# Performance work log

Hardware: AMD Instinct MI355X
Metric: run time of the kernel (lower is better)

## Reference

```python
import jax, jax.numpy as jnp
import numpy as np

# --- constants matching the torch module's default-camera / material / light setup ---
IMAGE_SIZE = 128
SCALE = 1.0
FOCAL = 12.0
R_MAT = jnp.array([[-1.0, 0.0, 0.0], [0.0, 1.0, 0.0], [0.0, 0.0, -1.0]], dtype=jnp.float32)
T_VEC = jnp.array([0.0, 0.0, 2.0 * SCALE], dtype=jnp.float32)
CAM_POS = jnp.array([0.0, 0.0, 2.0 * SCALE], dtype=jnp.float32)  # camera center in world coords
LIGHT_LOC = jnp.array([0.0, 1.0, 3.0], dtype=jnp.float32)
AMB_L, DIFF_L, SPEC_L = 0.5, 0.3, 0.2          # PointLights defaults
MAT_AMB, MAT_DIFF, MAT_SPEC = 1.0, 1.0, 0.6    # Materials(specular_color=0.6)
SHININESS = 10.0
TEXEL = jnp.array([142.0, 179.0, 247.0], dtype=jnp.float32) / 255.0  # uniform vertex color
BG = 1.0  # BlendParams background
EPS = 1e-8


def _normalize(v):
    return v / (jnp.linalg.norm(v, axis=-1, keepdims=True) + EPS)


def _render_one(verts, faces):
    """verts: [V,3] world space; faces: [F,3] int. Returns ([3,H,W] rgb*255, [1,H,W] alpha)."""
    H = W = IMAGE_SIZE
    # world -> view (PyTorch3D row-vector convention: x_view = x @ R + T)
    view = verts @ R_MAT + T_VEC              # [V,3]
    z = view[:, 2]                            # [V] view-space depth (>0 in front)
    ndc = FOCAL * view[:, :2] / z[:, None]    # [V,2] perspective projection to NDC
    tri = ndc[faces]                          # [F,3,2]
    tz = z[faces]                             # [F,3]

    # pixel centers in NDC (PyTorch3D: +x left, +y up)
    xs = 1.0 - (2.0 * jnp.arange(W) + 1.0) / W
    ys = 1.0 - (2.0 * jnp.arange(H) + 1.0) / H
    gy, gx = jnp.meshgrid(ys, xs, indexing='ij')
    px = gx.reshape(-1).astype(jnp.float32)   # [P]
    py = gy.reshape(-1).astype(jnp.float32)   # [P]

    v0, v1, v2 = tri[:, 0], tri[:, 1], tri[:, 2]   # [F,2]

    def edge(a, b):  # signed area cross(b-a, p-a) for all pixels -> [P,F]
        return ((b[:, 0] - a[:, 0])[None] * (py[:, None] - a[:, 1][None])
                - (b[:, 1] - a[:, 1])[None] * (px[:, None] - a[:, 0][None]))

    area = ((v1[:, 0] - v0[:, 0]) * (v2[:, 1] - v0[:, 1])
            - (v1[:, 1] - v0[:, 1]) * (v2[:, 0] - v0[:, 0]))   # [F]
    area_safe = jnp.where(jnp.abs(area) < EPS, EPS, area)
    b0 = edge(v1, v2) / area_safe             # [P,F]
    b1 = edge(v2, v0) / area_safe
    b2 = 1.0 - b0 - b1
    inside = (b0 >= 0) & (b1 >= 0) & (b2 >= 0) & (jnp.abs(area) > EPS)[None]

    # perspective-correct interpolated depth: z_pix = 1 / sum_i(b_i / z_i)
    S = b0 / tz[:, 0] + b1 / tz[:, 1] + b2 / tz[:, 2]
    depth = jnp.where(inside & (S > EPS), 1.0 / jnp.maximum(S, EPS), jnp.inf)
    fidx = jnp.argmin(depth, axis=1)          # [P] z-buffer winner (faces_per_pixel=1)
    hit = jnp.isfinite(jnp.min(depth, axis=1))

    # --- recompute barycentrics only for the winning face per pixel (cheap, [P]) ---
    f = faces[fidx]                           # [P,3]
    tv = ndc[f]                               # [P,3,2]
    tzp = z[f]                                # [P,3]
    a0, a1, a2 = tv[:, 0], tv[:, 1], tv[:, 2]

    def edge_p(a, b):
        return (b[:, 0] - a[:, 0]) * (py - a[:, 1]) - (b[:, 1] - a[:, 1]) * (px - a[:, 0])

    ar = (a1[:, 0] - a0[:, 0]) * (a2[:, 1] - a0[:, 1]) - (a1[:, 1] - a0[:, 1]) * (a2[:, 0] - a0[:, 0])
    ar = jnp.where(jnp.abs(ar) < EPS, EPS, ar)
    bb0 = edge_p(a1, a2) / ar
    bb1 = edge_p(a2, a0) / ar
    bb2 = 1.0 - bb0 - bb1
    w = jnp.stack([bb0 / tzp[:, 0], bb1 / tzp[:, 1], bb2 / tzp[:, 2]], axis=-1)
    pc = w / (jnp.sum(w, axis=-1, keepdims=True) + EPS)   # [P,3] perspective-correct barycentrics

    # --- vertex normals (world space) ---
    fv = verts[faces]                         # [F,3,3]
    fn = jnp.cross(fv[:, 1] - fv[:, 0], fv[:, 2] - fv[:, 0])  # [F,3]
    vn = (jnp.zeros_like(verts)
          .at[faces[:, 0]].add(fn)
          .at[faces[:, 1]].add(fn)
          .at[faces[:, 2]].add(fn))
    vn = _normalize(vn)

    # --- interpolate position/normal, Phong shade ---
    pos = jnp.einsum('pk,pkd->pd', pc, verts[f])   # [P,3]
    nrm = _normalize(jnp.einsum('pk,pkd->pd', pc, vn[f]))
    l = _normalize(LIGHT_LOC - pos)
    vdir = _normalize(CAM_POS - pos)
    ndl = jax.nn.relu(jnp.sum(nrm * l, axis=-1))          # [P]
    refl = 2.0 * jnp.sum(nrm * l, axis=-1, keepdims=True) * nrm - l
    spec_cos = jax.nn.relu(jnp.sum(refl * vdir, axis=-1))
    ambient = AMB_L * MAT_AMB
    diffuse = DIFF_L * MAT_DIFF * ndl
    specular = SPEC_L * MAT_SPEC * spec_cos ** SHININESS
    color = TEXEL[None] * (ambient + diffuse[:, None]) + specular[:, None]

    rgb = jnp.where(hit[:, None], color, BG)              # hard blend with white bg
    alpha = hit.astype(verts.dtype)
    img = rgb.reshape(H, W, 3).transpose(2, 0, 1) * 255.0  # [3,H,W]
    a = alpha.reshape(1, H, W)
    return img, a


def setup_inputs() -> dict:
    key = jax.random.key(0)
    k1, k2 = jax.random.split(key)
    B, V, F = 2, 1300, 2500
    vertices = jax.random.normal(k1, (B, V, 3), dtype=jnp.float32) * 0.05  # head-scale mesh near origin
    faces = jax.random.randint(k2, (F, 3), 0, V, dtype=jnp.int32)
    return {"vertices": vertices, "faces": faces}


def reference(vertices, faces):
    # ori_size == image_size, so the area-interpolation in the torch module is the identity.
    images, alphas = jax.lax.map(lambda v: _render_one(v, faces), vertices)
    return images, alphas
```

## Files before the change

kernel.cpp:

```cpp
#include <hip/hip_runtime.h>
#include <math.h>

#pragma clang fp contract(off)

#define IMG_H 128
#define IMG_W 128
#define HW (IMG_H * IMG_W)
#define NB 2
#define NV 1300
#define NF 2500
#define EPSF 1e-8f
#define NCHUNK 32
#define CHUNK ((NF + NCHUNK - 1) / NCHUNK)
#define NREG 128
#define NBLK (NREG * NB * NCHUNK)

#define OFF_FACE 31232
#define OFF_DBUF 351488

#define DINIT 0x7F800000FFFFFFFFull

__global__ __launch_bounds__(256) void k_face(const float* __restrict__ verts,
                                              const int* __restrict__ faces,
                                              float* __restrict__ vn,
                                              float4* __restrict__ face) {
    int i = blockIdx.x * 256 + threadIdx.x;
    if (i >= NB * NF) return;
    int b = i / NF;
    int f = i - b * NF;
    int i0 = faces[f * 3 + 0];
    int i1 = faces[f * 3 + 1];
    int i2 = faces[f * 3 + 2];
    const float* wv = verts + (size_t)b * NV * 3;
    float v0x = wv[i0 * 3 + 0], v0y = wv[i0 * 3 + 1], v0z = wv[i0 * 3 + 2];
    float v1x = wv[i1 * 3 + 0], v1y = wv[i1 * 3 + 1], v1z = wv[i1 * 3 + 2];
    float v2x = wv[i2 * 3 + 0], v2y = wv[i2 * 3 + 1], v2z = wv[i2 * 3 + 2];
    float z0 = 2.0f - v0z, z1 = 2.0f - v1z, z2 = 2.0f - v2z;
    float p0x = (12.0f * (-v0x)) / z0, p0y = (12.0f * v0y) / z0;
    float p1x = (12.0f * (-v1x)) / z1, p1y = (12.0f * v1y) / z1;
    float p2x = (12.0f * (-v2x)) / z2, p2y = (12.0f * v2y) / z2;

    float t1 = (p1x - p0x) * (p2y - p0y);
    float t2 = (p1y - p0y) * (p2x - p0x);
    float area = t1 - t2;
    float aabs = fabsf(area);
    float area_safe = (aabs < EPSF) ? EPSF : area;
    bool valid = aabs > EPSF;
    float minx, maxx, miny, maxy;
    if (valid) {
        minx = fminf(p0x, fminf(p1x, p2x)) - 1e-3f;
        maxx = fmaxf(p0x, fmaxf(p1x, p2x)) + 1e-3f;
        miny = fminf(p0y, fminf(p1y, p2y)) - 1e-3f;
        maxy = fmaxf(p0y, fmaxf(p1y, p2y)) + 1e-3f;
    } else {
        minx = 1e30f; maxx = -1e30f; miny = 1e30f; maxy = -1e30f;
    }
    int o = (b * NF + f) * 4;
    face[o + 0] = make_float4(p2x - p1x, p2y - p1y, p1x, p1y);
    face[o + 1] = make_float4(p0x - p2x, p0y - p2y, p2x, p2y);
    face[o + 2] = make_float4(area_safe, z0, z1, z2);
    face[o + 3] = make_float4(minx, maxx, miny, maxy);

    float ax = v1x - v0x, ay = v1y - v0y, az = v1z - v0z;
    float bx = v2x - v0x, by = v2y - v0y, bz = v2z - v0z;
    float fnx = ay * bz - az * by;
    float fny = az * bx - ax * bz;
    float fnz = ax * by - ay * bx;
    float* vnb = vn + (size_t)b * NV * 3;
    atomicAdd(&vnb[i0 * 3 + 0], fnx);
    atomicAdd(&vnb[i0 * 3 + 1], fny);
    atomicAdd(&vnb[i0 * 3 + 2], fnz);
    atomicAdd(&vnb[i1 * 3 + 0], fnx);
    atomicAdd(&vnb[i1 * 3 + 1], fny);
    atomicAdd(&vnb[i1 * 3 + 2], fnz);
    atomicAdd(&vnb[i2 * 3 + 0], fnx);
    atomicAdd(&vnb[i2 * 3 + 1], fny);
    atomicAdd(&vnb[i2 * 3 + 2], fnz);
}

__global__ __launch_bounds__(128) void k_raster(const float4* __restrict__ face,
                                                unsigned long long* __restrict__ dbuf) {
    __shared__ float4 sface[CHUNK * 4];
    __shared__ int sidx[CHUNK];
    __shared__ unsigned short swl[2][CHUNK];
    __shared__ int sbase[2];
    __shared__ int sbaseA[2];
    __shared__ int sbaseB[2];

    int bx = blockIdx.x;
    int chunk = bx & (NCHUNK - 1);
    int tmp = bx >> 5;
    int b = tmp & 1;
    int reg = tmp >> 1;
    int r0 = (reg >> 3) * 8;
    int c0 = (reg & 7) * 16;
    int f0 = chunk * CHUNK;
    int nf = NF - f0; if (nf > CHUNK) nf = CHUNK;

    float txmax   = 1.0f - (2.0f * (float)c0 + 1.0f) / 128.0f;
    float txmid_h = 1.0f - (2.0f * (float)(c0 + 7) + 1.0f) / 128.0f;
    float txmid_l = 1.0f - (2.0f * (float)(c0 + 8) + 1.0f) / 128.0f;
    float txmin   = 1.0f - (2.0f * (float)(c0 + 15) + 1.0f) / 128.0f;
    float tymax = 1.0f - (2.0f * (float)r0 + 1.0f) / 128.0f;
    float tymin = 1.0f - (2.0f * (float)(r0 + 7) + 1.0f) / 128.0f;

    const float4* fb = face + (size_t)b * NF * 4;
    int t = threadIdx.x;
    int wid = t >> 6, lid = t & 63;
    bool pass = false, pA = false, pB = false;
    float4 bb;
    if (t < nf) {
        bb = fb[(f0 + t) * 4 + 3];
        bool yok = (bb.w >= tymin) && (bb.z <= tymax);
        pA = yok && (bb.y >= txmid_h) && (bb.x <= txmax);
        pB = yok && (bb.y >= txmin) && (bb.x <= txmid_l);
        pass = pA || pB;
    }
    unsigned long long m  = __ballot(pass);
    unsigned long long mA = __ballot(pA);
    unsigned long long mB = __ballot(pB);
    if (lid == 0) {
        sbase[wid]  = __popcll(m);
        sbaseA[wid] = __popcll(mA);
        sbaseB[wid] = __popcll(mB);
    }
    __syncthreads();
    if (pass) {
        unsigned long long lt = (1ull << lid) - 1ull;
        int pos = (wid ? sbase[0] : 0) + __popcll(m & lt);
        sface[pos * 4 + 0] = fb[(f0 + t) * 4 + 0];
        sface[pos * 4 + 1] = fb[(f0 + t) * 4 + 1];
        sface[pos * 4 + 2] = fb[(f0 + t) * 4 + 2];
        sface[pos * 4 + 3] = bb;
        sidx[pos] = f0 + t;
        if (pA) swl[0][(wid ? sbaseA[0] : 0) + __popcll(mA & lt)] = (unsigned short)pos;
        if (pB) swl[1][(wid ? sbaseB[0] : 0) + __popcll(mB & lt)] = (unsigned short)pos;
    }
    __syncthreads();
    int cnt = wid ? (sbaseB[0] + sbaseB[1]) : (sbaseA[0] + sbaseA[1]);

    int r = r0 + (lid >> 3);
    int c = c0 + wid * 8 + (lid & 7);
    int p = r * IMG_W + c;
    float px = 1.0f - (2.0f * (float)c + 1.0f) / 128.0f;
    float py = 1.0f - (2.0f * (float)r + 1.0f) / 128.0f;

    unsigned long long best = DINIT;
    for (int j = 0; j < cnt; ++j) {
        int jj = swl[wid][j];
        float4 fbb = sface[jj * 4 + 3];
        if (px >= fbb.x && px <= fbb.y && py >= fbb.z && py <= fbb.w) {
            float4 E0 = sface[jj * 4 + 0];
            float4 E1 = sface[jj * 4 + 1];
            float4 FD = sface[jj * 4 + 2];
            float u1 = E0.x * (py - E0.w);
            float u2 = E0.y * (px - E0.z);
            float e0 = u1 - u2;
            float u3 = E1.x * (py - E1.w);
            float u4 = E1.y * (px - E1.z);
            float e1 = u3 - u4;
            float as = FD.x;
            bool ok = (as > 0.0f) ? (e0 >= 0.0f && e1 >= 0.0f)
                                  : (e0 <= 0.0f && e1 <= 0.0f);
            if (ok) {
                float b0 = e0 / as;
                float b1 = e1 / as;
                float b2 = (1.0f - b0) - b1;
                if (b2 >= 0.0f) {
                    float S = ((b0 / FD.y) + (b1 / FD.z)) + (b2 / FD.w);
                    if (S > EPSF) {
                        float depth = 1.0f / fmaxf(S, EPSF);
                        unsigned long long pk =
                            ((unsigned long long)__float_as_uint(depth) << 32) |
                            (unsigned)sidx[jj];
                        if (pk < best) best = pk;
                    }
                }
            }
        }
    }
    dbuf[((size_t)chunk * NB + b) * HW + p] = best;
}

__global__ __launch_bounds__(256) void k_shade(const float* __restrict__ verts,
                                               const int* __restrict__ faces,
                                               const float* __restrict__ vn,
                                               const unsigned long long* __restrict__ dbuf,
                                               float* __restrict__ out) {
    int i = blockIdx.x * 256 + threadIdx.x;
    int b = i >> 14;
    int p = i & (HW - 1);
    unsigned long long pk = DINIT;
    for (int k = 0; k < NCHUNK; ++k) {
        unsigned long long v = dbuf[((size_t)k * NB + b) * HW + p];
        if (v < pk) pk = v;
    }
    unsigned dbits = (unsigned)(pk >> 32);
    bool hit = dbits < 0x7F800000u;
    float cr = 255.0f, cg = 255.0f, cb = 255.0f, alpha = 0.0f;
    if (hit) {
        alpha = 1.0f;
        int f = (int)(unsigned)(pk & 0xFFFFFFFFull);
        int row = p >> 7;
        int col = p & 127;
        float px = 1.0f - (2.0f * (float)col + 1.0f) / 128.0f;
        float py = 1.0f - (2.0f * (float)row + 1.0f) / 128.0f;
        int i0 = faces[f * 3 + 0];
        int i1 = faces[f * 3 + 1];
        int i2 = faces[f * 3 + 2];
        const float* wv = verts + (size_t)b * NV * 3;
        float v0x = wv[i0 * 3 + 0], v0y = wv[i0 * 3 + 1], v0z = wv[i0 * 3 + 2];
        float v1x = wv[i1 * 3 + 0], v1y = wv[i1 * 3 + 1], v1z = wv[i1 * 3 + 2];
        float v2x = wv[i2 * 3 + 0], v2y = wv[i2 * 3 + 1], v2z = wv[i2 * 3 + 2];
        float z0 = 2.0f - v0z, z1 = 2.0f - v1z, z2 = 2.0f - v2z;
        float a0x = (12.0f * (-v0x)) / z0, a0y = (12.0f * v0y) / z0;
        float a1x = (12.0f * (-v1x)) / z1, a1y = (12.0f * v1y) / z1;
        float a2x = (12.0f * (-v2x)) / z2, a2y = (12.0f * v2y) / z2;

        float t1 = (a1x - a0x) * (a2y - a0y);
        float t2 = (a1y - a0y) * (a2x - a0x);
        float ar = t1 - t2;
        ar = (fabsf(ar) < EPSF) ? EPSF : ar;
        float u1 = (a2x - a1x) * (py - a1y);
        float u2 = (a2y - a1y) * (px - a1x);
        float bb0 = (u1 - u2) / ar;
        float u3 = (a0x - a2x) * (py - a2y);
        float u4 = (a0y - a2y) * (px - a2x);
        float bb1 = (u3 - u4) / ar;
        float bb2 = (1.0f - bb0) - bb1;
        float w0 = bb0 / z0;
        float w1 = bb1 / z1;
        float w2 = bb2 / z2;
        float denom = ((w0 + w1) + w2) + EPSF;
        float pc0 = w0 / denom;
        float pc1 = w1 / denom;
        float pc2 = w2 / denom;

        float posx = (pc0 * v0x + pc1 * v1x) + pc2 * v2x;
        float posy = (pc0 * v0y + pc1 * v1y) + pc2 * v2y;
        float posz = (pc0 * v0z + pc1 * v1z) + pc2 * v2z;

        const float* vnb = vn + (size_t)b * NV * 3;
        float n0x = vnb[i0 * 3 + 0], n0y = vnb[i0 * 3 + 1], n0z = vnb[i0 * 3 + 2];
        float n1x = vnb[i1 * 3 + 0], n1y = vnb[i1 * 3 + 1], n1z = vnb[i1 * 3 + 2];
        float n2x = vnb[i2 * 3 + 0], n2y = vnb[i2 * 3 + 1], n2z = vnb[i2 * 3 + 2];
        float in0 = 1.0f / (sqrtf(n0x * n0x + n0y * n0y + n0z * n0z) + EPSF);
        float in1 = 1.0f / (sqrtf(n1x * n1x + n1y * n1y + n1z * n1z) + EPSF);
        float in2 = 1.0f / (sqrtf(n2x * n2x + n2y * n2y + n2z * n2z) + EPSF);
        n0x *= in0; n0y *= in0; n0z *= in0;
        n1x *= in1; n1y *= in1; n1z *= in1;
        n2x *= in2; n2y *= in2; n2z *= in2;
        float nx = (pc0 * n0x + pc1 * n1x) + pc2 * n2x;
        float ny = (pc0 * n0y + pc1 * n1y) + pc2 * n2y;
        float nz = (pc0 * n0z + pc1 * n1z) + pc2 * n2z;
        float inn = 1.0f / (sqrtf(nx * nx + ny * ny + nz * nz) + EPSF);
        nx *= inn; ny *= inn; nz *= inn;

        float lx = 0.0f - posx, ly = 1.0f - posy, lz = 3.0f - posz;
        float iln = 1.0f / (sqrtf(lx * lx + ly * ly + lz * lz) + EPSF);
        lx *= iln; ly *= iln; lz *= iln;
        float vx = 0.0f - posx, vy = 0.0f - posy, vz = 2.0f - posz;
        float ivn = 1.0f / (sqrtf(vx * vx + vy * vy + vz * vz) + EPSF);
        vx *= ivn; vy *= ivn; vz *= ivn;

        float ndl = nx * lx + ny * ly + nz * lz;
        float ndlr = fmaxf(ndl, 0.0f);
        float rx = 2.0f * ndl * nx - lx;
        float ry = 2.0f * ndl * ny - ly;
        float rz = 2.0f * ndl * nz - lz;
        float sc = fmaxf(rx * vx + ry * vy + rz * vz, 0.0f);
        float spec = 0.2f * 0.6f * powf(sc, 10.0f);
        float shade = 0.5f * 1.0f + 0.3f * 1.0f * ndlr;
        cr = ((142.0f / 255.0f) * shade + spec) * 255.0f;
        cg = ((179.0f / 255.0f) * shade + spec) * 255.0f;
        cb = ((247.0f / 255.0f) * shade + spec) * 255.0f;
    }
    float* img = out + (size_t)b * 3 * HW;
    img[0 * HW + p] = cr;
    img[1 * HW + p] = cg;
    img[2 * HW + p] = cb;
    out[(size_t)NB * 3 * HW + (size_t)b * HW + p] = alpha;
}

extern "C" void kernel_launch(void* const* d_in, const int* in_sizes, int n_in,
                              void* d_out, int out_size, void* d_ws, size_t ws_size,
                              hipStream_t stream) {
    const float* verts = (const float*)d_in[0];
    const int* faces = (const int*)d_in[1];
    char* ws = (char*)d_ws;
    float* vn = (float*)(ws + 0);
    float4* face = (float4*)(ws + OFF_FACE);
    unsigned long long* dbuf = (unsigned long long*)(ws + OFF_DBUF);
    float* out = (float*)d_out;

    hipMemsetAsync(vn, 0, NB * NV * 3 * sizeof(float), stream);
    k_face<<<(NB * NF + 255) / 256, 256, 0, stream>>>(verts, faces, vn, face);
    k_raster<<<NBLK, 128, 0, stream>>>(face, dbuf);
    k_shade<<<(NB * HW) / 256, 256, 0, stream>>>(verts, faces, vn, dbuf, out);
}
```

Measured before the change: 104.1 us.

## Cull faces per tile with edge-function bounds and merge depths via atomicMin

Tightens per-tile face culling in the raster kernel. It evaluates edge-function bounds over each half-tile rectangle and drops faces whose triangle cannot overlap it, using a small tolerance. It also replaces the per-chunk depth buffer and the 32-way min reduction in the shade kernel with 64-bit atomicMin into a single buffer, initialised by an extra memset. This cuts shared-memory candidates, dbuf traffic and the shade reduction, at the cost of atomic contention and an extra memset launch.

```diff
diff --git a/kernel.cpp b/kernel.cpp
--- a/kernel.cpp
+++ b/kernel.cpp
@@ -18,7 +18,7 @@
 #define OFF_FACE 31232
 #define OFF_DBUF 351488
 
-#define DINIT 0x7F800000FFFFFFFFull
+#define DINIT 0xFFFFFFFFFFFFFFFFull
 
 __global__ __launch_bounds__(256) void k_face(const float* __restrict__ verts,
                                               const int* __restrict__ faces,
@@ -108,12 +108,45 @@
     int t = threadIdx.x;
     int wid = t >> 6, lid = t & 63;
     bool pass = false, pA = false, pB = false;
-    float4 bb;
+    float4 bb, E0, E1, FD;
     if (t < nf) {
         bb = fb[(f0 + t) * 4 + 3];
         bool yok = (bb.w >= tymin) && (bb.z <= tymax);
         pA = yok && (bb.y >= txmid_h) && (bb.x <= txmax);
         pB = yok && (bb.y >= txmin) && (bb.x <= txmid_l);
+        if (pA || pB) {
+            E0 = fb[(f0 + t) * 4 + 0];
+            E1 = fb[(f0 + t) * 4 + 1];
+            FD = fb[(f0 + t) * 4 + 2];
+            float as = FD.x;
+            float u0l = E0.x * (tymin - E0.w), u0h = E0.x * (tymax - E0.w);
+            float u0mn = fminf(u0l, u0h), u0mx = fmaxf(u0l, u0h);
+            float u1l = E1.x * (tymin - E1.w), u1h = E1.x * (tymax - E1.w);
+            float u1mn = fminf(u1l, u1h), u1mx = fmaxf(u1l, u1h);
+            float v0al = E0.y * (txmid_h - E0.z), v0ah = E0.y * (txmax - E0.z);
+            float v0amn = fminf(v0al, v0ah), v0amx = fmaxf(v0al, v0ah);
+            float v1al = E1.y * (txmid_h - E1.z), v1ah = E1.y * (txmax - E1.z);
+            float v1amn = fminf(v1al, v1ah), v1amx = fmaxf(v1al, v1ah);
+            float v0bl = E0.y * (txmin - E0.z), v0bh = E0.y * (txmid_l - E0.z);
+            float v0bmn = fminf(v0bl, v0bh), v0bmx = fmaxf(v0bl, v0bh);
+            float v1bl = E1.y * (txmin - E1.z), v1bh = E1.y * (txmid_l - E1.z);
+            float v1bmn = fminf(v1bl, v1bh), v1bmx = fmaxf(v1bl, v1bh);
+            float e0amx = u0mx - v0amn, e0amn = u0mn - v0amx;
+            float e1amx = u1mx - v1amn, e1amn = u1mn - v1amx;
+            float e0bmx = u0mx - v0bmn, e0bmn = u0mn - v0bmx;
+            float e1bmx = u1mx - v1bmn, e1bmn = u1mn - v1bmx;
+            const float DL = 1e-4f;
+            bool okA, okB;
+            if (as > 0.0f) {
+                okA = (e0amx >= -DL) && (e1amx >= -DL) && (((as - e0amn) - e1amn) >= -DL);
+                okB = (e0bmx >= -DL) && (e1bmx >= -DL) && (((as - e0bmn) - e1bmn) >= -DL);
+            } else {
+                okA = (e0amn <= DL) && (e1amn <= DL) && (((as - e0amx) - e1amx) <= DL);
+                okB = (e0bmn <= DL) && (e1bmn <= DL) && (((as - e0bmx) - e1bmx) <= DL);
+            }
+            pA = pA && okA;
+            pB = pB && okB;
+        }
         pass = pA || pB;
     }
     unsigned long long m  = __ballot(pass);
@@ -128,9 +161,9 @@
     if (pass) {
         unsigned long long lt = (1ull << lid) - 1ull;
         int pos = (wid ? sbase[0] : 0) + __popcll(m & lt);
-        sface[pos * 4 + 0] = fb[(f0 + t) * 4 + 0];
-        sface[pos * 4 + 1] = fb[(f0 + t) * 4 + 1];
-        sface[pos * 4 + 2] = fb[(f0 + t) * 4 + 2];
+        sface[pos * 4 + 0] = E0;
+        sface[pos * 4 + 1] = E1;
+        sface[pos * 4 + 2] = FD;
         sface[pos * 4 + 3] = bb;
         sidx[pos] = f0 + t;
         if (pA) swl[0][(wid ? sbaseA[0] : 0) + __popcll(mA & lt)] = (unsigned short)pos;
@@ -150,16 +183,16 @@
         int jj = swl[wid][j];
         float4 fbb = sface[jj * 4 + 3];
         if (px >= fbb.x && px <= fbb.y && py >= fbb.z && py <= fbb.w) {
-            float4 E0 = sface[jj * 4 + 0];
-            float4 E1 = sface[jj * 4 + 1];
-            float4 FD = sface[jj * 4 + 2];
-            float u1 = E0.x * (py - E0.w);
-            float u2 = E0.y * (px - E0.z);
+            float4 e0v = sface[jj * 4 + 0];
+            float4 e1v = sface[jj * 4 + 1];
+            float4 fdv = sface[jj * 4 + 2];
+            float u1 = e0v.x * (py - e0v.w);
+            float u2 = e0v.y * (px - e0v.z);
             float e0 = u1 - u2;
-            float u3 = E1.x * (py - E1.w);
-            float u4 = E1.y * (px - E1.z);
+            float u3 = e1v.x * (py - e1v.w);
+            float u4 = e1v.y * (px - e1v.z);
             float e1 = u3 - u4;
-            float as = FD.x;
+            float as = fdv.x;
             bool ok = (as > 0.0f) ? (e0 >= 0.0f && e1 >= 0.0f)
                                   : (e0 <= 0.0f && e1 <= 0.0f);
             if (ok) {
@@ -167,7 +200,7 @@
                 float b1 = e1 / as;
                 float b2 = (1.0f - b0) - b1;
                 if (b2 >= 0.0f) {
-                    float S = ((b0 / FD.y) + (b1 / FD.z)) + (b2 / FD.w);
+                    float S = ((b0 / fdv.y) + (b1 / fdv.z)) + (b2 / fdv.w);
                     if (S > EPSF) {
                         float depth = 1.0f / fmaxf(S, EPSF);
                         unsigned long long pk =
@@ -179,7 +212,8 @@
             }
         }
     }
-    dbuf[((size_t)chunk * NB + b) * HW + p] = best;
+    if (best != DINIT)
+        atomicMin(&dbuf[(size_t)b * HW + p], best);
 }
 
 __global__ __launch_bounds__(256) void k_shade(const float* __restrict__ verts,
@@ -190,11 +224,7 @@
     int i = blockIdx.x * 256 + threadIdx.x;
     int b = i >> 14;
     int p = i & (HW - 1);
-    unsigned long long pk = DINIT;
-    for (int k = 0; k < NCHUNK; ++k) {
-        unsigned long long v = dbuf[((size_t)k * NB + b) * HW + p];
-        if (v < pk) pk = v;
-    }
+    unsigned long long pk = dbuf[(size_t)b * HW + p];
     unsigned dbits = (unsigned)(pk >> 32);
     bool hit = dbits < 0x7F800000u;
     float cr = 255.0f, cg = 255.0f, cb = 255.0f, alpha = 0.0f;
@@ -294,6 +324,7 @@
     float* out = (float*)d_out;
 
     hipMemsetAsync(vn, 0, NB * NV * 3 * sizeof(float), stream);
+    hipMemsetAsync(dbuf, 0xFF, (size_t)NB * HW * sizeof(unsigned long long), stream);
     k_face<<<(NB * NF + 255) / 256, 256, 0, stream>>>(verts, faces, vn, face);
     k_raster<<<NBLK, 128, 0, stream>>>(face, dbuf);
     k_shade<<<(NB * HW) / 256, 256, 0, stream>>>(verts, faces, vn, dbuf, out);
```

After: 111.2 us. 6.8% more time.

## Cull faces per wave with conservative edge test and shrink shade block size

Applied to the files above, without the earlier changes.

The rasterizer now has each 64-lane wave build its own face list for its 8x8 pixel tile. A face is kept only if its bounding box overlaps the tile and its edge functions, evaluated conservatively at the tile corners, cannot rule it out. This drops the block-wide ballot/prefix and index indirection and removes the two __syncthreads, so each wave loops over fewer candidate faces. Faces are loaded per wave in 64-face batches. The shade kernel is relaunched with 64-thread blocks instead of 256. The conservative test uses a fixed 1e-4 tolerance, so precision mistakes could wrongly cull faces near edges.

```diff
diff --git a/kernel.cpp b/kernel.cpp
--- a/kernel.cpp
+++ b/kernel.cpp
@@ -80,12 +80,8 @@
 
 __global__ __launch_bounds__(128) void k_raster(const float4* __restrict__ face,
                                                 unsigned long long* __restrict__ dbuf) {
-    __shared__ float4 sface[CHUNK * 4];
-    __shared__ int sidx[CHUNK];
-    __shared__ unsigned short swl[2][CHUNK];
-    __shared__ int sbase[2];
-    __shared__ int sbaseA[2];
-    __shared__ int sbaseB[2];
+    __shared__ float4 sface[2][CHUNK * 4];
+    __shared__ unsigned short sidx[2][CHUNK];
 
     int bx = blockIdx.x;
     int chunk = bx & (NCHUNK - 1);
@@ -97,69 +93,82 @@
     int f0 = chunk * CHUNK;
     int nf = NF - f0; if (nf > CHUNK) nf = CHUNK;
 
-    float txmax   = 1.0f - (2.0f * (float)c0 + 1.0f) / 128.0f;
-    float txmid_h = 1.0f - (2.0f * (float)(c0 + 7) + 1.0f) / 128.0f;
-    float txmid_l = 1.0f - (2.0f * (float)(c0 + 8) + 1.0f) / 128.0f;
-    float txmin   = 1.0f - (2.0f * (float)(c0 + 15) + 1.0f) / 128.0f;
-    float tymax = 1.0f - (2.0f * (float)r0 + 1.0f) / 128.0f;
-    float tymin = 1.0f - (2.0f * (float)(r0 + 7) + 1.0f) / 128.0f;
-
-    const float4* fb = face + (size_t)b * NF * 4;
     int t = threadIdx.x;
     int wid = t >> 6, lid = t & 63;
-    bool pass = false, pA = false, pB = false;
-    float4 bb;
-    if (t < nf) {
-        bb = fb[(f0 + t) * 4 + 3];
-        bool yok = (bb.w >= tymin) && (bb.z <= tymax);
-        pA = yok && (bb.y >= txmid_h) && (bb.x <= txmax);
-        pB = yok && (bb.y >= txmin) && (bb.x <= txmid_l);
-        pass = pA || pB;
-    }
-    unsigned long long m  = __ballot(pass);
-    unsigned long long mA = __ballot(pA);
-    unsigned long long mB = __ballot(pB);
-    if (lid == 0) {
-        sbase[wid]  = __popcll(m);
-        sbaseA[wid] = __popcll(mA);
-        sbaseB[wid] = __popcll(mB);
-    }
-    __syncthreads();
-    if (pass) {
-        unsigned long long lt = (1ull << lid) - 1ull;
-        int pos = (wid ? sbase[0] : 0) + __popcll(m & lt);
-        sface[pos * 4 + 0] = fb[(f0 + t) * 4 + 0];
-        sface[pos * 4 + 1] = fb[(f0 + t) * 4 + 1];
-        sface[pos * 4 + 2] = fb[(f0 + t) * 4 + 2];
-        sface[pos * 4 + 3] = bb;
-        sidx[pos] = f0 + t;
-        if (pA) swl[0][(wid ? sbaseA[0] : 0) + __popcll(mA & lt)] = (unsigned short)pos;
-        if (pB) swl[1][(wid ? sbaseB[0] : 0) + __popcll(mB & lt)] = (unsigned short)pos;
-    }
-    __syncthreads();
-    int cnt = wid ? (sbaseB[0] + sbaseB[1]) : (sbaseA[0] + sbaseA[1]);
+    int cw0 = c0 + wid * 8;
+
+    float txhi = 1.0f - (2.0f * (float)cw0 + 1.0f) / 128.0f;
+    float txlo = 1.0f - (2.0f * (float)(cw0 + 7) + 1.0f) / 128.0f;
+    float tyhi = 1.0f - (2.0f * (float)r0 + 1.0f) / 128.0f;
+    float tylo = 1.0f - (2.0f * (float)(r0 + 7) + 1.0f) / 128.0f;
+
+    const float4* fb = face + (size_t)b * NF * 4;
+
+    int cnt = 0;
+    for (int base = 0; base < nf; base += 64) {
+        int tt = base + lid;
+        bool pass = false;
+        float4 bb, E0, E1, FD;
+        if (tt < nf) {
+            bb = fb[(f0 + tt) * 4 + 3];
+            pass = (bb.y >= txlo) && (bb.x <= txhi) && (bb.w >= tylo) && (bb.z <= tyhi);
+            if (pass) {
+                E0 = fb[(f0 + tt) * 4 + 0];
+                E1 = fb[(f0 + tt) * 4 + 1];
+                FD = fb[(f0 + tt) * 4 + 2];
+                float as = FD.x;
+                float u0l = E0.x * (tylo - E0.w), u0h = E0.x * (tyhi - E0.w);
+                float u0mn = fminf(u0l, u0h), u0mx = fmaxf(u0l, u0h);
+                float u1l = E1.x * (tylo - E1.w), u1h = E1.x * (tyhi - E1.w);
+                float u1mn = fminf(u1l, u1h), u1mx = fmaxf(u1l, u1h);
+                float v0l = E0.y * (txlo - E0.z), v0h = E0.y * (txhi - E0.z);
+                float v0mn = fminf(v0l, v0h), v0mx = fmaxf(v0l, v0h);
+                float v1l = E1.y * (txlo - E1.z), v1h = E1.y * (txhi - E1.z);
+                float v1mn = fminf(v1l, v1h), v1mx = fmaxf(v1l, v1h);
+                float e0mx = u0mx - v0mn, e0mn = u0mn - v0mx;
+                float e1mx = u1mx - v1mn, e1mn = u1mn - v1mx;
+                const float DL = 1e-4f;
+                bool ok;
+                if (as > 0.0f) {
+                    ok = (e0mx >= -DL) && (e1mx >= -DL) && (((as - e0mn) - e1mn) >= -DL);
+                } else {
+                    ok = (e0mn <= DL) && (e1mn <= DL) && (((as - e0mx) - e1mx) <= DL);
+                }
+                pass = ok;
+            }
+        }
+        unsigned long long m = __ballot(pass);
+        if (pass) {
+            int pos = cnt + __popcll(m & ((1ull << lid) - 1ull));
+            sface[wid][pos * 4 + 0] = E0;
+            sface[wid][pos * 4 + 1] = E1;
+            sface[wid][pos * 4 + 2] = FD;
+            sface[wid][pos * 4 + 3] = bb;
+            sidx[wid][pos] = (unsigned short)tt;
+        }
+        cnt += __popcll(m);
+    }
 
     int r = r0 + (lid >> 3);
-    int c = c0 + wid * 8 + (lid & 7);
+    int c = cw0 + (lid & 7);
     int p = r * IMG_W + c;
     float px = 1.0f - (2.0f * (float)c + 1.0f) / 128.0f;
     float py = 1.0f - (2.0f * (float)r + 1.0f) / 128.0f;
 
     unsigned long long best = DINIT;
     for (int j = 0; j < cnt; ++j) {
-        int jj = swl[wid][j];
-        float4 fbb = sface[jj * 4 + 3];
+        float4 fbb = sface[wid][j * 4 + 3];
         if (px >= fbb.x && px <= fbb.y && py >= fbb.z && py <= fbb.w) {
-            float4 E0 = sface[jj * 4 + 0];
-            float4 E1 = sface[jj * 4 + 1];
-            float4 FD = sface[jj * 4 + 2];
-            float u1 = E0.x * (py - E0.w);
-            float u2 = E0.y * (px - E0.z);
+            float4 e0v = sface[wid][j * 4 + 0];
+            float4 e1v = sface[wid][j * 4 + 1];
+            float4 fdv = sface[wid][j * 4 + 2];
+            float u1 = e0v.x * (py - e0v.w);
+            float u2 = e0v.y * (px - e0v.z);
             float e0 = u1 - u2;
-            float u3 = E1.x * (py - E1.w);
-            float u4 = E1.y * (px - E1.z);
+            float u3 = e1v.x * (py - e1v.w);
+            float u4 = e1v.y * (px - e1v.z);
             float e1 = u3 - u4;
-            float as = FD.x;
+            float as = fdv.x;
             bool ok = (as > 0.0f) ? (e0 >= 0.0f && e1 >= 0.0f)
                                   : (e0 <= 0.0f && e1 <= 0.0f);
             if (ok) {
@@ -167,12 +176,12 @@
                 float b1 = e1 / as;
                 float b2 = (1.0f - b0) - b1;
                 if (b2 >= 0.0f) {
-                    float S = ((b0 / FD.y) + (b1 / FD.z)) + (b2 / FD.w);
+                    float S = ((b0 / fdv.y) + (b1 / fdv.z)) + (b2 / fdv.w);
                     if (S > EPSF) {
                         float depth = 1.0f / fmaxf(S, EPSF);
                         unsigned long long pk =
                             ((unsigned long long)__float_as_uint(depth) << 32) |
-                            (unsigned)sidx[jj];
+                            (unsigned)(f0 + sidx[wid][j]);
                         if (pk < best) best = pk;
                     }
                 }
@@ -182,12 +191,12 @@
     dbuf[((size_t)chunk * NB + b) * HW + p] = best;
 }
 
-__global__ __launch_bounds__(256) void k_shade(const float* __restrict__ verts,
-                                               const int* __restrict__ faces,
-                                               const float* __restrict__ vn,
-                                               const unsigned long long* __restrict__ dbuf,
-                                               float* __restrict__ out) {
-    int i = blockIdx.x * 256 + threadIdx.x;
+__global__ __launch_bounds__(64) void k_shade(const float* __restrict__ verts,
+                                              const int* __restrict__ faces,
+                                              const float* __restrict__ vn,
+                                              const unsigned long long* __restrict__ dbuf,
+                                              float* __restrict__ out) {
+    int i = blockIdx.x * 64 + threadIdx.x;
     int b = i >> 14;
     int p = i & (HW - 1);
     unsigned long long pk = DINIT;
@@ -296,5 +305,5 @@
     hipMemsetAsync(vn, 0, NB * NV * 3 * sizeof(float), stream);
     k_face<<<(NB * NF + 255) / 256, 256, 0, stream>>>(verts, faces, vn, face);
     k_raster<<<NBLK, 128, 0, stream>>>(face, dbuf);
-    k_shade<<<(NB * HW) / 256, 256, 0, stream>>>(verts, faces, vn, dbuf, out);
+    k_shade<<<(NB * HW) / 64, 64, 0, stream>>>(verts, faces, vn, dbuf, out);
 }
```

Result: faster. 101.8 us (-2.2%).
